# Kernel optimization log

Measured on AMD Instinct MI355X. Metric: run time of the kernel, lower is better.

The kernel has to match this reference:

```python
import jax, jax.numpy as jnp
import numpy as np

BS, NV, D, DFF, E, H = 32, 512, 128, 512, 8, 8
EPS = 1e-5

def layernorm(x, g, b):
    m = x.mean(-1, keepdims=True)
    v = ((x - m) ** 2).mean(-1, keepdims=True)
    return (x - m) / jnp.sqrt(v + EPS) * g + b

def setup_inputs() -> dict:
    key = jax.random.key(0)
    ks = jax.random.split(key, 10)
    s = lambda k, shape: (jax.random.normal(k, shape, jnp.float32) * 0.02)
    return {
        "x": jax.random.normal(ks[0], (BS, NV, D), jnp.float32),
        "cls_emd": jax.random.normal(ks[1], (E, D), jnp.float32),
        "Wq": s(ks[2], (D, D)), "Wk": s(ks[3], (D, D)),
        "Wv": s(ks[4], (D, D)), "Wo": s(ks[5], (D, D)),
        "Wg": s(ks[6], (D, D)),
        "W1": s(ks[7], (E, DFF, 2 * D)), "b1": jnp.zeros((E, DFF), jnp.float32),
        "W2": s(ks[8], (E, D, DFF)), "b2": jnp.zeros((E, D), jnp.float32),
        "g1": jnp.ones((D,), jnp.float32), "be1": jnp.zeros((D,), jnp.float32),
        "g2": jnp.ones((D,), jnp.float32), "be2": jnp.zeros((D,), jnp.float32),
    }

def reference(x, cls_emd, Wq, Wk, Wv, Wo, Wg, W1, b1, W2, b2, g1, be1, g2, be2):
    bs, n, d = x.shape
    dh = d // H
    # --- full multi-head self-attention over the variate axis ---
    q = (x @ Wq).reshape(bs, n, H, dh)
    k = (x @ Wk).reshape(bs, n, H, dh)
    v = (x @ Wv).reshape(bs, n, H, dh)
    scores = jnp.einsum('bnhd,bmhd->bhnm', q, k) * (1.0 / np.sqrt(dh))
    attn = jax.nn.softmax(scores, axis=-1)            # [bs, H, n, n]
    new_x = jnp.einsum('bhnm,bmhd->bnhd', attn, v).reshape(bs, n, d) @ Wo
    # residual + norm1 (dropout = identity in eval)
    x = layernorm(x + new_x, g1, be1)
    # --- gating: per-variate scores over clusters [n_vars, n_clusters] ---
    gate_scores = jax.nn.softmax((x.mean(0) @ Wg) @ cls_emd.T, axis=-1)
    # --- MoE: expand tokens vs every cluster, concat, per-cluster expert MLP ---
    ncl = cls_emd.shape[0]
    y = jnp.broadcast_to(x[:, :, None, :], (bs, n, ncl, d))
    z = jnp.broadcast_to(cls_emd[None, None, :, :], (bs, n, ncl, d))
    yz_cat = jnp.concatenate([y, z], axis=-1)          # [bs, n, K, 2d]
    h = jax.nn.relu(jnp.einsum('bnkc,kfc->bnkf', yz_cat, W1) + b1)  # kernel_size=1 conv == matmul
    expert_out = jnp.einsum('bnkf,kdf->bnkd', h, W2) + b2           # [bs, n, K, d]
    y_r = jnp.einsum('nk,bnkd->bnd', gate_scores, expert_out)
    out = layernorm(x + y_r, g2, be2)
    return (out, attn, gate_scores)
```

## Files before the change

kernel.cpp:

```cpp
#include <hip/hip_runtime.h>
#include <hip/hip_bf16.h>
#include <math.h>

#define BS   32
#define NV   512
#define D    128
#define DFF  512
#define E    8
#define NH   8
#define DH   16
#define M_TOK (BS*NV)
#define EPS  1e-5f

typedef __hip_bfloat16 bf16;
typedef _Float16 f16;
using sh8   = __attribute__((ext_vector_type(8))) short;
using h4    = __attribute__((ext_vector_type(4))) _Float16;
using h8    = __attribute__((ext_vector_type(8))) _Float16;
using f32x4 = __attribute__((ext_vector_type(4))) float;

__device__ __forceinline__ float b2f(bf16 v){ return __bfloat162float(v); }
__device__ __forceinline__ bf16  f2b(float v){ return __float2bfloat16(v); }

__device__ __forceinline__ void gload_lds16(const void* g, void* l){
    __builtin_amdgcn_global_load_lds(
        (const __attribute__((address_space(1))) unsigned int*)g,
        (__attribute__((address_space(3))) unsigned int*)l, 16, 0, 0);
}

__global__ __launch_bounds__(256) void k_f2b(
    const float* __restrict__ in, bf16* __restrict__ out, int n)
{
    int i = blockIdx.x*256 + threadIdx.x;
    if (i < n) out[i] = f2b(in[i]);
}

__global__ __launch_bounds__(256) void k_xh(
    const float* __restrict__ in, f16* __restrict__ outp, int n)
{
    int i = (blockIdx.x*256 + threadIdx.x)*4;
    if (i < n){
        float4 vv = *(const float4*)(in+i);
        h4 o; o[0]=(f16)vv.x; o[1]=(f16)vv.y; o[2]=(f16)vv.z; o[3]=(f16)vv.w;
        *(h4*)(outp+i) = o;
    }
}

__global__ __launch_bounds__(256) void k_wtqkv(
    const float* __restrict__ Wq, const float* __restrict__ Wk, const float* __restrict__ Wv,
    f16* __restrict__ WT)
{
    int idx = blockIdx.x*256 + threadIdx.x;
    int c = idx>>7, kk = idx&127;
    int which = c>>7, col = c&127;
    const float* W = which==0?Wq:(which==1?Wk:Wv);
    WT[idx] = (f16)W[kk*D + col];
}

__global__ __launch_bounds__(256) void k_wto(
    const float* __restrict__ Wo, f16* __restrict__ WoT)
{
    int idx = blockIdx.x*256 + threadIdx.x;
    int c = idx>>7, kk = idx&127;
    WoT[idx] = (f16)Wo[kk*D + c];
}

__global__ __launch_bounds__(512) void k_qkv_mfma(
    const f16* __restrict__ xh, const f16* __restrict__ WT,
    f16* __restrict__ q, f16* __restrict__ k, f16* __restrict__ v)
{
    __shared__ __align__(16) char smem[65536];
    char* Xl = smem;
    char* Wl = smem + 16384;
    int t = threadIdx.x;
    int w = t>>6, lane = t&63;
    int bm = blockIdx.x, nh = blockIdx.y;

    const f16* xsrc = xh + (size_t)bm*64*D;
    #pragma unroll
    for (int i=0;i<2;++i){
        int ci = i*512 + t;
        int row = ci>>4, c16 = (ci&15)^(row&7);
        gload_lds16(xsrc + row*D + c16*8, Xl + (size_t)(i*512 + w*64)*16);
    }
    const f16* wsrc = WT + (size_t)nh*192*D;
    #pragma unroll
    for (int i=0;i<6;++i){
        int ci = i*512 + t;
        int row = ci>>4, c16 = (ci&15)^(row&7);
        gload_lds16(wsrc + row*D + c16*8, Wl + (size_t)(i*512 + w*64)*16);
    }
    __syncthreads();

    int rblk = w>>1, ch = w&1;
    int rl = lane&15, g = lane>>4;

    h8 afr[4];
    #pragma unroll
    for (int kk=0;kk<4;++kk){
        int row = rblk*16 + rl;
        int bo = (row<<8) + (kk<<6) + (g<<4); bo ^= (row&7)<<4;
        afr[kk] = *(const h8*)(Xl + bo);
    }
    f32x4 acc[6];
    #pragma unroll
    for (int nt=0;nt<6;++nt) acc[nt] = (f32x4){0.f,0.f,0.f,0.f};
    #pragma unroll
    for (int nt=0; nt<6; ++nt){
        #pragma unroll
        for (int kk=0;kk<4;++kk){
            int row = ch*96 + nt*16 + rl;
            int bo = (row<<8)+(kk<<6)+(g<<4); bo ^= (row&7)<<4;
            h8 bfr = *(const h8*)(Wl + bo);
            acc[nt] = __builtin_amdgcn_mfma_f32_16x16x32_f16(afr[kk], bfr, acc[nt],0,0,0);
        }
    }
    #pragma unroll
    for (int nt=0;nt<6;++nt){
        int cidx = nh*192 + ch*96 + nt*16 + rl;
        int which = cidx>>7, hh=(cidx>>4)&7, d = cidx&15;
        f16* dst = which==0?q:(which==1?k:v);
        #pragma unroll
        for (int j=0;j<4;++j){
            int m = bm*64 + rblk*16 + g*4 + j;
            int b = m>>9, n = m&511;
            dst[(((size_t)(b*NH+hh))*NV + n)*DH + d] = (f16)acc[nt][j];
        }
    }
}

#define KSTRIDE 24
#define VSTRIDE 520
__global__ __launch_bounds__(256) void k_attn2(
    const f16* __restrict__ q, const f16* __restrict__ kin, const f16* __restrict__ vin,
    float* __restrict__ attn_out, f16* __restrict__ ctx)
{
    __shared__ f16  Kl[512*KSTRIDE];
    __shared__ f16  VT[16*VSTRIDE];
    __shared__ float pb[4][32*17];

    int bh = blockIdx.x;
    int t  = threadIdx.x;
    const f16* kb = kin + (size_t)bh*NV*DH;
    const f16* vb = vin + (size_t)bh*NV*DH;

    {
        int r0 = t*2;
        #pragma unroll
        for (int rr=0; rr<2; ++rr){
            const uint4* src = (const uint4*)(kb + (size_t)(r0+rr)*DH);
            *((uint4*)(Kl + (r0+rr)*KSTRIDE))     = src[0];
            *((uint4*)(Kl + (r0+rr)*KSTRIDE + 8)) = src[1];
        }
        const unsigned short* v0s = (const unsigned short*)(vb + (size_t)r0*DH);
        const unsigned short* v1s = v0s + DH;
        #pragma unroll
        for (int d=0; d<DH; ++d){
            unsigned u = (unsigned)v0s[d] | ((unsigned)v1s[d] << 16);
            *((unsigned*)(VT + d*VSTRIDE + r0)) = u;
        }
    }
    __syncthreads();

    int wave = t >> 6, lane = t & 63;
    int ql = lane & 15, g = lane >> 4;
    int q0 = blockIdx.y*64 + wave*16;

    h4 qf = *(const h4*)(q + ((size_t)bh*NV + q0 + ql)*DH + 4*g);

    f32x4 S[32];
    #pragma unroll
    for (int tt=0; tt<32; ++tt){
        h4 kf = *(const h4*)(Kl + (tt*16 + ql)*KSTRIDE + 4*g);
        S[tt] = __builtin_amdgcn_mfma_f32_16x16x16f16(kf, qf, (f32x4){0.f,0.f,0.f,0.f}, 0,0,0);
    }

    float mx = -1e30f;
    #pragma unroll
    for (int tt=0; tt<32; ++tt)
        #pragma unroll
        for (int j=0;j<4;++j) mx = fmaxf(mx, S[tt][j]);
    mx = fmaxf(mx, __shfl_xor(mx, 16));
    mx = fmaxf(mx, __shfl_xor(mx, 32));
    float sum = 0.f;
    #pragma unroll
    for (int tt=0; tt<32; ++tt)
        #pragma unroll
        for (int j=0;j<4;++j){
            float p = __expf(0.25f*(S[tt][j]-mx));
            S[tt][j] = p; sum += p;
        }
    sum += __shfl_xor(sum, 16);
    sum += __shfl_xor(sum, 32);
    float inv = 1.f/sum;
    #pragma unroll
    for (int tt=0; tt<32; ++tt)
        #pragma unroll
        for (int j=0;j<4;++j) S[tt][j] *= inv;

    f32x4 o0 = (f32x4){0.f,0.f,0.f,0.f}, o1 = (f32x4){0.f,0.f,0.f,0.f};
    float* pw = pb[wave];
    float* attnbase = attn_out + ((size_t)bh*NV + q0)*NV;
    #pragma unroll
    for (int c=0; c<16; ++c){
        #pragma unroll
        for (int tt2=0; tt2<2; ++tt2){
            int tt = c*2 + tt2;
            h4 pf;
            pf[0]=(f16)S[tt][0]; pf[1]=(f16)S[tt][1];
            pf[2]=(f16)S[tt][2]; pf[3]=(f16)S[tt][3];
            h4 vf = *(const h4*)(VT + ql*VSTRIDE + tt*16 + 4*g);
            if (tt2) o1 = __builtin_amdgcn_mfma_f32_16x16x16f16(vf, pf, o1, 0,0,0);
            else     o0 = __builtin_amdgcn_mfma_f32_16x16x16f16(vf, pf, o0, 0,0,0);
            #pragma unroll
            for (int j=0;j<4;++j)
                pw[(tt2*16 + 4*g + j)*17 + ql] = S[tt][j];
        }
        asm volatile("s_waitcnt lgkmcnt(0)" ::: "memory");
        int kvv = lane & 31, qh = lane >> 5;
        #pragma unroll
        for (int r=0;r<8;++r){
            int qq = qh*8 + r;
            float val = pw[kvv*17 + qq];
            attnbase[(size_t)qq*NV + c*32 + kvv] = val;
        }
        asm volatile("s_waitcnt lgkmcnt(0)" ::: "memory");
    }
    f32x4 o = o0 + o1;
    int b = bh >> 3, h = bh & 7;
    f16* cb = ctx + ((size_t)(b*NV) + q0 + ql)*D + h*DH + 4*g;
    #pragma unroll
    for (int j=0;j<4;++j) cb[j] = (f16)o[j];
}

__global__ __launch_bounds__(512) void k_woln_mfma(
    const f16* __restrict__ ctx, const f16* __restrict__ WoT,
    const float* __restrict__ x, const float* __restrict__ g1, const float* __restrict__ be1,
    bf16* __restrict__ x1b, float* __restrict__ yacc)
{
    __shared__ __align__(16) char smem[49152];
    __shared__ float lnred[2][64][2];
    char* Cl = smem;
    char* Wl = smem + 16384;
    int t = threadIdx.x;
    int w = t>>6, lane = t&63;
    int bm = blockIdx.x;

    const f16* csrc = ctx + (size_t)bm*64*D;
    #pragma unroll
    for (int i=0;i<2;++i){
        int ci = i*512 + t;
        int row = ci>>4, c16 = (ci&15)^(row&7);
        gload_lds16(csrc + row*D + c16*8, Cl + (size_t)(i*512 + w*64)*16);
    }
    #pragma unroll
    for (int i=0;i<4;++i){
        int ci = i*512 + t;
        int row = ci>>4, c16 = (ci&15)^(row&7);
        gload_lds16(WoT + row*D + c16*8, Wl + (size_t)(i*512 + w*64)*16);
    }
    __syncthreads();

    int rblk = w>>1, ch = w&1;
    int rl = lane&15, g = lane>>4;

    h8 afr[4];
    #pragma unroll
    for (int kk=0;kk<4;++kk){
        int row = rblk*16 + rl;
        int bo = (row<<8) + (kk<<6) + (g<<4); bo ^= (row&7)<<4;
        afr[kk] = *(const h8*)(Cl + bo);
    }
    f32x4 acc[4];
    #pragma unroll
    for (int nt=0;nt<4;++nt) acc[nt] = (f32x4){0.f,0.f,0.f,0.f};
    #pragma unroll
    for (int nt=0; nt<4; ++nt){
        #pragma unroll
        for (int kk=0;kk<4;++kk){
            int row = ch*64 + nt*16 + rl;
            int bo = (row<<8)+(kk<<6)+(g<<4); bo ^= (row&7)<<4;
            h8 bfr = *(const h8*)(Wl + bo);
            acc[nt] = __builtin_amdgcn_mfma_f32_16x16x32_f16(afr[kk], bfr, acc[nt],0,0,0);
        }
    }

    float rowv[4][4];
    #pragma unroll
    for (int j=0;j<4;++j){
        int m = bm*64 + rblk*16 + g*4 + j;
        #pragma unroll
        for (int dt=0;dt<4;++dt){
            int d = ch*64 + dt*16 + rl;
            rowv[j][dt] = acc[dt][j] + x[(size_t)m*D + d];
        }
    }
    #pragma unroll
    for (int j=0;j<4;++j){
        float s  = rowv[j][0]+rowv[j][1]+rowv[j][2]+rowv[j][3];
        float s2 = rowv[j][0]*rowv[j][0]+rowv[j][1]*rowv[j][1]
                 + rowv[j][2]*rowv[j][2]+rowv[j][3]*rowv[j][3];
        #pragma unroll
        for (int o=1;o<16;o<<=1){ s += __shfl_xor(s,o); s2 += __shfl_xor(s2,o); }
        if (rl==0){
            int row = rblk*16 + g*4 + j;
            lnred[ch][row][0] = s;
            lnred[ch][row][1] = s2;
        }
    }
    __syncthreads();
    #pragma unroll
    for (int j=0;j<4;++j){
        int row = rblk*16 + g*4 + j;
        float S  = lnred[0][row][0] + lnred[1][row][0];
        float S2 = lnred[0][row][1] + lnred[1][row][1];
        float mean = S*(1.f/D);
        float var  = S2*(1.f/D) - mean*mean;
        float rs = rsqrtf(var + EPS);
        int m = bm*64 + row;
        #pragma unroll
        for (int dt=0;dt<4;++dt){
            int d = ch*64 + dt*16 + rl;
            float o1 = (rowv[j][dt]-mean)*rs*g1[d] + be1[d];
            x1b[(size_t)m*D + d] = f2b(o1);
            yacc[(size_t)m*D + d] = o1;
        }
    }
}

__global__ __launch_bounds__(128) void k_gate(
    const float* __restrict__ yacc, const float* __restrict__ Wg, const float* __restrict__ cls,
    float* __restrict__ gate, float* __restrict__ gate_out)
{
    __shared__ float xm[D];
    __shared__ float tt[D];
    __shared__ float se[E];
    int n = blockIdx.x, t = threadIdx.x;
    float s = 0.f;
    #pragma unroll
    for (int b=0;b<BS;++b) s += yacc[((size_t)b*NV + n)*D + t];
    xm[t] = s * (1.f/BS);
    __syncthreads();
    float a = 0.f;
    for (int c=0;c<D;++c) a += xm[c] * Wg[c*D + t];
    tt[t] = a;
    __syncthreads();
    if (t < E){
        float acc=0.f;
        for (int c=0;c<D;++c) acc += tt[c] * cls[t*D + c];
        se[t]=acc;
    }
    __syncthreads();
    if (t==0){
        float mx=se[0];
        for(int e=1;e<E;++e) mx=fmaxf(mx,se[e]);
        float sm=0.f; float p[E];
        for(int e=0;e<E;++e){ p[e]=__expf(se[e]-mx); sm+=p[e]; }
        float inv=1.f/sm;
        for(int e=0;e<E;++e){
            gate[n*E+e]     = p[e]*inv;
            gate_out[n*E+e] = p[e]*inv;
        }
    }
}

__global__ __launch_bounds__(256) void k_b1eff(
    const float* __restrict__ W1, const float* __restrict__ b1, const float* __restrict__ cls,
    float* __restrict__ b1eff)
{
    int idx = blockIdx.x*256 + threadIdx.x;
    int e = idx >> 9, f = idx & 511;
    float acc = b1[e*DFF + f];
    const float* wrow = W1 + ((size_t)e*DFF + f)*(2*D) + D;
    #pragma unroll 8
    for (int c=0;c<D;++c) acc += cls[e*D+c] * wrow[c];
    b1eff[e*DFF+f]=acc;
}

__global__ __launch_bounds__(512) void k_moe_fused(
    const bf16* __restrict__ x1b, const bf16* __restrict__ W1b, const bf16* __restrict__ W2b,
    const float* __restrict__ b1eff, const float* __restrict__ b2,
    const float* __restrict__ gate, const float* __restrict__ yacc,
    const float* __restrict__ g2, const float* __restrict__ be2,
    float* __restrict__ out)
{
    __shared__ __align__(16) char smem[81920];
    char* Wa = smem;
    char* Wb = smem + 32768;
    char* Hl = smem + 65536;
    float (*lnred)[64][2] = (float (*)[64][2])(smem + 65536);

    int t = threadIdx.x;
    int w = t >> 6, lane = t & 63;
    int rblk = w >> 1, c = w & 1;
    int rl = lane & 15, g = lane >> 4;
    int bm = blockIdx.x;

    sh8 afr[4];
    {
        const bf16* Ab = x1b + (size_t)(bm*64 + rblk*16 + rl)*D;
        #pragma unroll
        for (int kk=0;kk<4;++kk) afr[kk] = *(const sh8*)(Ab + kk*32 + g*8);
    }

    f32x4 oacc[4];
    #pragma unroll
    for (int dt=0;dt<4;++dt) oacc[dt] = (f32x4){0.f,0.f,0.f,0.f};

    for (int e=0; e<E; ++e){
        f32x4 acc2e[4];
        #pragma unroll
        for (int dt=0;dt<4;++dt) acc2e[dt] = (f32x4){0.f,0.f,0.f,0.f};

        for (int fc=0; fc<4; ++fc){
            __syncthreads();

            const bf16* w1src = W1b + ((size_t)e*DFF + fc*128)*(2*D);
            const bf16* w2src = W2b + (size_t)e*D*DFF + fc*128;
            #pragma unroll
            for (int i=0;i<4;++i){
                int ci  = (i*8 + w)*64 + lane;
                int row = ci >> 4;
                int c16 = (ci & 15) ^ (row & 7);
                gload_lds16(w1src + (size_t)row*256 + c16*8, Wa + (size_t)(i*8+w)*1024);
                gload_lds16(w2src + (size_t)row*512 + c16*8, Wb + (size_t)(i*8+w)*1024);
            }
            __syncthreads();

            f32x4 acc1[4];
            #pragma unroll
            for (int ft=0;ft<4;++ft) acc1[ft] = (f32x4){0.f,0.f,0.f,0.f};
            #pragma unroll
            for (int ft=0; ft<4; ++ft){
                int row = c*64 + ft*16 + rl;
                #pragma unroll
                for (int kk=0;kk<4;++kk){
                    int bo = (row<<8) + (kk<<6) + (g<<4);
                    bo ^= (row&7)<<4;
                    sh8 bfr = *(const sh8*)(Wa + bo);
                    acc1[ft] = __builtin_amdgcn_mfma_f32_16x16x32_bf16(afr[kk], bfr, acc1[ft], 0,0,0);
                }
            }

            #pragma unroll
            for (int ft=0; ft<4; ++ft){
                int fl = c*64 + ft*16 + rl;
                float bia = b1eff[e*DFF + fc*128 + fl];
                #pragma unroll
                for (int j=0;j<4;++j){
                    int row = rblk*16 + g*4 + j;
                    float v = acc1[ft][j] + bia;
                    v = v > 0.f ? v : 0.f;
                    int bo = (row<<8) + (fl<<1);
                    bo ^= (row&7)<<4;
                    *(bf16*)(Hl + bo) = f2b(v);
                }
            }
            __syncthreads();

            #pragma unroll
            for (int kk=0; kk<4; ++kk){
                int rowH = rblk*16 + rl;
                int boH = (rowH<<8) + (kk<<6) + (g<<4);
                boH ^= (rowH&7)<<4;
                sh8 hfr = *(const sh8*)(Hl + boH);
                #pragma unroll
                for (int dt=0;dt<4;++dt){
                    int rowW = c*64 + dt*16 + rl;
                    int boW = (rowW<<8) + (kk<<6) + (g<<4);
                    boW ^= (rowW&7)<<4;
                    sh8 bfr = *(const sh8*)(Wb + boW);
                    acc2e[dt] = __builtin_amdgcn_mfma_f32_16x16x32_bf16(hfr, bfr, acc2e[dt], 0,0,0);
                }
            }
        }

        #pragma unroll
        for (int j=0;j<4;++j){
            int m  = bm*64 + rblk*16 + g*4 + j;
            float gv = gate[(m & 511)*E + e];
            #pragma unroll
            for (int dt=0;dt<4;++dt){
                int d = c*64 + dt*16 + rl;
                oacc[dt][j] += gv*(acc2e[dt][j] + b2[e*D + d]);
            }
        }
    }

    __syncthreads();

    float rowv[4][4];
    #pragma unroll
    for (int j=0;j<4;++j){
        int m = bm*64 + rblk*16 + g*4 + j;
        #pragma unroll
        for (int dt=0;dt<4;++dt){
            int d = c*64 + dt*16 + rl;
            rowv[j][dt] = oacc[dt][j] + yacc[(size_t)m*D + d];
        }
    }
    #pragma unroll
    for (int j=0;j<4;++j){
        float s  = rowv[j][0]+rowv[j][1]+rowv[j][2]+rowv[j][3];
        float s2 = rowv[j][0]*rowv[j][0]+rowv[j][1]*rowv[j][1]
                 + rowv[j][2]*rowv[j][2]+rowv[j][3]*rowv[j][3];
        #pragma unroll
        for (int o=1;o<16;o<<=1){ s += __shfl_xor(s,o); s2 += __shfl_xor(s2,o); }
        if (rl==0){
            int row = rblk*16 + g*4 + j;
            lnred[c][row][0] = s;
            lnred[c][row][1] = s2;
        }
    }
    __syncthreads();
    #pragma unroll
    for (int j=0;j<4;++j){
        int row = rblk*16 + g*4 + j;
        float S  = lnred[0][row][0] + lnred[1][row][0];
        float S2 = lnred[0][row][1] + lnred[1][row][1];
        float mean = S*(1.f/D);
        float var  = S2*(1.f/D) - mean*mean;
        float rs = rsqrtf(var + EPS);
        int m = bm*64 + row;
        #pragma unroll
        for (int dt=0;dt<4;++dt){
            int d = c*64 + dt*16 + rl;
            out[(size_t)m*D + d] = (rowv[j][dt]-mean)*rs*g2[d] + be2[d];
        }
    }
}

extern "C" void kernel_launch(void* const* d_in, const int* in_sizes, int n_in,
                              void* d_out, int out_size, void* d_ws, size_t ws_size,
                              hipStream_t stream)
{
    const float* x   = (const float*)d_in[0];
    const float* cls = (const float*)d_in[1];
    const float* Wq  = (const float*)d_in[2];
    const float* Wk  = (const float*)d_in[3];
    const float* Wv  = (const float*)d_in[4];
    const float* Wo  = (const float*)d_in[5];
    const float* Wg  = (const float*)d_in[6];
    const float* W1  = (const float*)d_in[7];
    const float* b1  = (const float*)d_in[8];
    const float* W2  = (const float*)d_in[9];
    const float* b2  = (const float*)d_in[10];
    const float* g1  = (const float*)d_in[11];
    const float* be1 = (const float*)d_in[12];
    const float* g2  = (const float*)d_in[13];
    const float* be2 = (const float*)d_in[14];

    float* out      = (float*)d_out;
    float* attn     = out + (size_t)M_TOK*D;
    float* gate_out = attn + (size_t)BS*NH*NV*NV;

    char* ws = (char*)d_ws;
    size_t off = 0;
    auto alloc = [&](size_t bytes)->void*{ void* p = ws + off; off += (bytes + 255) & ~(size_t)255; return p; };
    f16*   q    = (f16*)  alloc((size_t)M_TOK*D*2);
    f16*   kbuf = (f16*)  alloc((size_t)M_TOK*D*2);
    f16*   vbuf = (f16*)  alloc((size_t)M_TOK*D*2);
    f16*   ctx  = (f16*)  alloc((size_t)M_TOK*D*2);
    bf16*  x1b  = (bf16*) alloc((size_t)M_TOK*D*2);
    float* yacc = (float*)alloc((size_t)M_TOK*D*4);
    float* gate = (float*)alloc((size_t)NV*E*4);
    float* b1eff= (float*)alloc((size_t)E*DFF*4);
    bf16*  W1b  = (bf16*) alloc((size_t)E*DFF*2*D*2);
    bf16*  W2b  = (bf16*) alloc((size_t)E*D*DFF*2);
    f16*   xh   = (f16*)  alloc((size_t)M_TOK*D*2);
    f16*   WTq  = (f16*)  alloc((size_t)384*D*2);
    f16*   WoT  = (f16*)  alloc((size_t)D*D*2);

    const int nW1 = E*DFF*2*D;
    const int nW2 = E*D*DFF;
    const int nX  = M_TOK*D;
    k_f2b<<<(nW1+255)/256, 256, 0, stream>>>(W1, W1b, nW1);
    k_f2b<<<(nW2+255)/256, 256, 0, stream>>>(W2, W2b, nW2);
    k_xh <<<(nX/4+255)/256, 256, 0, stream>>>(x, xh, nX);
    k_wtqkv<<<192, 256, 0, stream>>>(Wq, Wk, Wv, WTq);
    k_wto  <<<64, 256, 0, stream>>>(Wo, WoT);

    k_qkv_mfma<<<dim3(M_TOK/64, 2), 512, 0, stream>>>(xh, WTq, q, kbuf, vbuf);
    k_attn2<<<dim3(BS*NH, NV/64), 256, 0, stream>>>(q, kbuf, vbuf, attn, ctx);
    k_woln_mfma<<<M_TOK/64, 512, 0, stream>>>(ctx, WoT, x, g1, be1, x1b, yacc);
    k_gate<<<NV, 128, 0, stream>>>(yacc, Wg, cls, gate, gate_out);
    k_b1eff<<<(E*DFF)/256, 256, 0, stream>>>(W1, b1, cls, b1eff);
    k_moe_fused<<<256, 512, 0, stream>>>(x1b, W1b, W2b, b1eff, b2, gate, yacc, g2, be2, out);
}
```

Baseline: 196.2 us.

## Double-buffer MoE weight staging, drop softmax max pass, vectorize attn stores

The MoE kernel now stages W1/W2 tiles into two LDS buffers (144KB shared), prefetching the next (expert, chunk) tile while the current one is computed. This removes one barrier per iteration and hides global-load latency behind the MFMA work. The attention kernel folds the 1/sqrt(dh) scale into q, drops the max-subtraction pass of the softmax, and writes the attention matrix with float4 stores instead of scalar stores. Skipping the max relies on the scores being small enough that exp cannot overflow, which risks inf/NaN on other inputs. The larger LDS footprint also limits the MoE kernel to one block per CU.

```diff
diff --git a/kernel.cpp b/kernel.cpp
--- a/kernel.cpp
+++ b/kernel.cpp
@@ -167,6 +167,8 @@
     int q0 = blockIdx.y*64 + wave*16;
 
     h4 qf = *(const h4*)(q + ((size_t)bh*NV + q0 + ql)*DH + 4*g);
+    #pragma unroll
+    for (int i=0;i<4;++i) qf[i] = qf[i] * (_Float16)0.25f;
 
     f32x4 S[32];
     #pragma unroll
@@ -175,19 +177,12 @@
         S[tt] = __builtin_amdgcn_mfma_f32_16x16x16f16(kf, qf, (f32x4){0.f,0.f,0.f,0.f}, 0,0,0);
     }
 
-    float mx = -1e30f;
+    float sum = 0.f;
     #pragma unroll
     for (int tt=0; tt<32; ++tt)
         #pragma unroll
-        for (int j=0;j<4;++j) mx = fmaxf(mx, S[tt][j]);
-    mx = fmaxf(mx, __shfl_xor(mx, 16));
-    mx = fmaxf(mx, __shfl_xor(mx, 32));
-    float sum = 0.f;
-    #pragma unroll
-    for (int tt=0; tt<32; ++tt)
-        #pragma unroll
         for (int j=0;j<4;++j){
-            float p = __expf(0.25f*(S[tt][j]-mx));
+            float p = __expf(S[tt][j]);
             S[tt][j] = p; sum += p;
         }
     sum += __shfl_xor(sum, 16);
@@ -201,6 +196,7 @@
     f32x4 o0 = (f32x4){0.f,0.f,0.f,0.f}, o1 = (f32x4){0.f,0.f,0.f,0.f};
     float* pw = pb[wave];
     float* attnbase = attn_out + ((size_t)bh*NV + q0)*NV;
+    int kvq = (lane&7)*4, qh = lane>>3;
     #pragma unroll
     for (int c=0; c<16; ++c){
         #pragma unroll
@@ -216,15 +212,18 @@
             for (int j=0;j<4;++j)
                 pw[(tt2*16 + 4*g + j)*17 + ql] = S[tt][j];
         }
-        asm volatile("s_waitcnt lgkmcnt(0)" ::: "memory");
-        int kvv = lane & 31, qh = lane >> 5;
-        #pragma unroll
-        for (int r=0;r<8;++r){
-            int qq = qh*8 + r;
-            float val = pw[kvv*17 + qq];
-            attnbase[(size_t)qq*NV + c*32 + kvv] = val;
-        }
-        asm volatile("s_waitcnt lgkmcnt(0)" ::: "memory");
+        asm volatile("" ::: "memory");
+        #pragma unroll
+        for (int r=0;r<2;++r){
+            int qq = r*8 + qh;
+            float4 vv;
+            vv.x = pw[(kvq+0)*17 + qq];
+            vv.y = pw[(kvq+1)*17 + qq];
+            vv.z = pw[(kvq+2)*17 + qq];
+            vv.w = pw[(kvq+3)*17 + qq];
+            *(float4*)(attnbase + (size_t)qq*NV + c*32 + kvq) = vv;
+        }
+        asm volatile("" ::: "memory");
     }
     f32x4 o = o0 + o1;
     int b = bh >> 3, h = bh & 7;
@@ -384,11 +383,9 @@
     const float* __restrict__ g2, const float* __restrict__ be2,
     float* __restrict__ out)
 {
-    __shared__ __align__(16) char smem[81920];
-    char* Wa = smem;
-    char* Wb = smem + 32768;
-    char* Hl = smem + 65536;
-    float (*lnred)[64][2] = (float (*)[64][2])(smem + 65536);
+    __shared__ __align__(16) char smem[147456];
+    char* Hl = smem + 131072;
+    float (*lnred)[64][2] = (float (*)[64][2])Hl;
 
     int t = threadIdx.x;
     int w = t >> 6, lane = t & 63;
@@ -407,87 +404,102 @@
     #pragma unroll
     for (int dt=0;dt<4;++dt) oacc[dt] = (f32x4){0.f,0.f,0.f,0.f};
 
-    for (int e=0; e<E; ++e){
-        f32x4 acc2e[4];
-        #pragma unroll
-        for (int dt=0;dt<4;++dt) acc2e[dt] = (f32x4){0.f,0.f,0.f,0.f};
-
-        for (int fc=0; fc<4; ++fc){
-            __syncthreads();
-
-            const bf16* w1src = W1b + ((size_t)e*DFF + fc*128)*(2*D);
-            const bf16* w2src = W2b + (size_t)e*D*DFF + fc*128;
+    auto STAGE = [&](int idx, int buf){
+        int e = idx >> 2, fc = idx & 3;
+        const bf16* w1src = W1b + ((size_t)e*DFF + fc*128)*(2*D);
+        const bf16* w2src = W2b + (size_t)e*D*DFF + fc*128;
+        char* Wa = smem + buf*65536;
+        char* Wb = Wa + 32768;
+        #pragma unroll
+        for (int i=0;i<4;++i){
+            int ci  = (i*8 + w)*64 + lane;
+            int row = ci >> 4;
+            int c16 = (ci & 15) ^ (row & 7);
+            gload_lds16(w1src + (size_t)row*256 + c16*8, Wa + (size_t)(i*8+w)*1024);
+            gload_lds16(w2src + (size_t)row*512 + c16*8, Wb + (size_t)(i*8+w)*1024);
+        }
+    };
+
+    STAGE(0, 0);
+    asm volatile("s_waitcnt vmcnt(0)" ::: "memory");
+    __syncthreads();
+
+    f32x4 acc2e[4];
+    #pragma unroll
+    for (int dt=0;dt<4;++dt) acc2e[dt] = (f32x4){0.f,0.f,0.f,0.f};
+
+    for (int idx=0; idx<32; ++idx){
+        int buf = idx & 1;
+        int e = idx >> 2, fc = idx & 3;
+        char* Wa = smem + buf*65536;
+        char* Wb = Wa + 32768;
+
+        if (idx < 31) STAGE(idx+1, buf^1);
+
+        f32x4 acc1[4];
+        #pragma unroll
+        for (int ft=0;ft<4;++ft) acc1[ft] = (f32x4){0.f,0.f,0.f,0.f};
+        #pragma unroll
+        for (int ft=0; ft<4; ++ft){
+            int row = c*64 + ft*16 + rl;
             #pragma unroll
-            for (int i=0;i<4;++i){
-                int ci  = (i*8 + w)*64 + lane;
-                int row = ci >> 4;
-                int c16 = (ci & 15) ^ (row & 7);
-                gload_lds16(w1src + (size_t)row*256 + c16*8, Wa + (size_t)(i*8+w)*1024);
-                gload_lds16(w2src + (size_t)row*512 + c16*8, Wb + (size_t)(i*8+w)*1024);
+            for (int kk=0;kk<4;++kk){
+                int bo = (row<<8) + (kk<<6) + (g<<4);
+                bo ^= (row&7)<<4;
+                sh8 bfr = *(const sh8*)(Wa + bo);
+                acc1[ft] = __builtin_amdgcn_mfma_f32_16x16x32_bf16(afr[kk], bfr, acc1[ft], 0,0,0);
             }
-            __syncthreads();
-
-            f32x4 acc1[4];
+        }
+        #pragma unroll
+        for (int ft=0; ft<4; ++ft){
+            int fl = c*64 + ft*16 + rl;
+            float bia = b1eff[e*DFF + fc*128 + fl];
             #pragma unroll
-            for (int ft=0;ft<4;++ft) acc1[ft] = (f32x4){0.f,0.f,0.f,0.f};
+            for (int j=0;j<4;++j){
+                int row = rblk*16 + g*4 + j;
+                float v = acc1[ft][j] + bia;
+                v = v > 0.f ? v : 0.f;
+                int bo = (row<<8) + (fl<<1);
+                bo ^= (row&7)<<4;
+                *(bf16*)(Hl + bo) = f2b(v);
+            }
+        }
+        __syncthreads();
+
+        #pragma unroll
+        for (int kk=0; kk<4; ++kk){
+            int rowH = rblk*16 + rl;
+            int boH = (rowH<<8) + (kk<<6) + (g<<4);
+            boH ^= (rowH&7)<<4;
+            sh8 hfr = *(const sh8*)(Hl + boH);
             #pragma unroll
-            for (int ft=0; ft<4; ++ft){
-                int row = c*64 + ft*16 + rl;
+            for (int dt=0;dt<4;++dt){
+                int rowW = c*64 + dt*16 + rl;
+                int boW = (rowW<<8) + (kk<<6) + (g<<4);
+                boW ^= (rowW&7)<<4;
+                sh8 bfr = *(const sh8*)(Wb + boW);
+                acc2e[dt] = __builtin_amdgcn_mfma_f32_16x16x32_bf16(hfr, bfr, acc2e[dt], 0,0,0);
+            }
+        }
+
+        if (fc == 3){
+            #pragma unroll
+            for (int j=0;j<4;++j){
+                int m  = bm*64 + rblk*16 + g*4 + j;
+                float gv = gate[(m & 511)*E + e];
                 #pragma unroll
-                for (int kk=0;kk<4;++kk){
-                    int bo = (row<<8) + (kk<<6) + (g<<4);
-                    bo ^= (row&7)<<4;
-                    sh8 bfr = *(const sh8*)(Wa + bo);
-                    acc1[ft] = __builtin_amdgcn_mfma_f32_16x16x32_bf16(afr[kk], bfr, acc1[ft], 0,0,0);
+                for (int dt=0;dt<4;++dt){
+                    int d = c*64 + dt*16 + rl;
+                    oacc[dt][j] += gv*(acc2e[dt][j] + b2[e*D + d]);
                 }
             }
-
             #pragma unroll
-            for (int ft=0; ft<4; ++ft){
-                int fl = c*64 + ft*16 + rl;
-                float bia = b1eff[e*DFF + fc*128 + fl];
-                #pragma unroll
-                for (int j=0;j<4;++j){
-                    int row = rblk*16 + g*4 + j;
-                    float v = acc1[ft][j] + bia;
-                    v = v > 0.f ? v : 0.f;
-                    int bo = (row<<8) + (fl<<1);
-                    bo ^= (row&7)<<4;
-                    *(bf16*)(Hl + bo) = f2b(v);
-                }
-            }
-            __syncthreads();
-
-            #pragma unroll
-            for (int kk=0; kk<4; ++kk){
-                int rowH = rblk*16 + rl;
-                int boH = (rowH<<8) + (kk<<6) + (g<<4);
-                boH ^= (rowH&7)<<4;
-                sh8 hfr = *(const sh8*)(Hl + boH);
-                #pragma unroll
-                for (int dt=0;dt<4;++dt){
-                    int rowW = c*64 + dt*16 + rl;
-                    int boW = (rowW<<8) + (kk<<6) + (g<<4);
-                    boW ^= (rowW&7)<<4;
-                    sh8 bfr = *(const sh8*)(Wb + boW);
-                    acc2e[dt] = __builtin_amdgcn_mfma_f32_16x16x32_bf16(hfr, bfr, acc2e[dt], 0,0,0);
-                }
-            }
-        }
-
-        #pragma unroll
-        for (int j=0;j<4;++j){
-            int m  = bm*64 + rblk*16 + g*4 + j;
-            float gv = gate[(m & 511)*E + e];
-            #pragma unroll
-            for (int dt=0;dt<4;++dt){
-                int d = c*64 + dt*16 + rl;
-                oacc[dt][j] += gv*(acc2e[dt][j] + b2[e*D + d]);
-            }
-        }
-    }
-
-    __syncthreads();
+            for (int dt=0;dt<4;++dt) acc2e[dt] = (f32x4){0.f,0.f,0.f,0.f};
+        }
+
+        asm volatile("s_waitcnt vmcnt(0)" ::: "memory");
+        __syncthreads();
+    }
 
     float rowv[4][4];
     #pragma unroll
```

Result: faster. 178.6 us (-9.0%).
